# Kernel tuning notes

Hardware: AMD Instinct MI355X
Metric: run time of the kernel (lower is better)

The kernel has to match this reference:

```python
import jax, jax.numpy as jnp
import numpy as np

EMB, ENC, HID, L, V = 512, 1024, 1024, 2, 32000
INTER = (HID + ENC + EMB + V) // 16  # 2160, matches int((h+i+e+v)/16)
B, S_ENC, T_DEC = 32, 64, 64


def setup_inputs() -> dict:
    key = jax.random.key(0)
    ks = jax.random.split(key, 24)
    w = lambda k, shape, fan: (jax.random.normal(k, shape, jnp.float32) / np.sqrt(fan))
    inp = {
        'enc_output': jax.random.normal(ks[0], (B, S_ENC, ENC), jnp.float32),
        'encoder_mask': jnp.ones((B, S_ENC), jnp.int32),
        'y_input': jax.random.randint(ks[1], (B, T_DEC), 0, V),
        'dec_h0': jax.random.normal(ks[2], (L, B, HID), jnp.float32),
        'dec_c0': jax.random.normal(ks[3], (L, B, HID), jnp.float32),
        # embedding table
        'emb_table': w(ks[4], (V, EMB), EMB),
        # additive (Bahdanau) attention params: score = v^T tanh(We*enc + Wd*h_top)
        'We': w(ks[5], (ENC, HID), ENC),
        'Wd': w(ks[6], (HID, HID), HID),
        'v': w(ks[7], (HID,), HID),
        # 2-layer LSTM (torch gate order i,f,g,o)
        'W_ih0': w(ks[8], (4 * HID, EMB + ENC), EMB + ENC),
        'W_hh0': w(ks[9], (4 * HID, HID), HID),
        'b_ih0': jnp.zeros((4 * HID,), jnp.float32),
        'b_hh0': jnp.zeros((4 * HID,), jnp.float32),
        'W_ih1': w(ks[10], (4 * HID, HID), HID),
        'W_hh1': w(ks[11], (4 * HID, HID), HID),
        'b_ih1': jnp.zeros((4 * HID,), jnp.float32),
        'b_hh1': jnp.zeros((4 * HID,), jnp.float32),
        # output MLP head
        'out_W': w(ks[12], (INTER, HID + ENC + EMB), HID + ENC + EMB),
        'out_b': jnp.zeros((INTER,), jnp.float32),
        'sm_W': w(ks[13], (V, INTER), INTER),
        'sm_b': jnp.zeros((V,), jnp.float32),
        'teacher_forcing_ratio': 1,
    }
    return inp


def _lstm_cell(x, h, c, W_ih, W_hh, b_ih, b_hh):
    g = x @ W_ih.T + b_ih + h @ W_hh.T + b_hh
    i, f, gg, o = jnp.split(g, 4, axis=-1)
    c2 = jax.nn.sigmoid(f) * c + jax.nn.sigmoid(i) * jnp.tanh(gg)
    h2 = jax.nn.sigmoid(o) * jnp.tanh(c2)
    return h2, c2


def reference(enc_output, encoder_mask, y_input, dec_h0, dec_c0, emb_table,
              We, Wd, v, W_ih0, W_hh0, b_ih0, b_hh0, W_ih1, W_hh1, b_ih1, b_hh1,
              out_W, out_b, sm_W, sm_b, teacher_forcing_ratio):
    # teacher_forcing_ratio == 1 -> always use ground-truth previous token
    embs = emb_table[y_input[:, :-1]]            # [B, T-1, E] (dropout p=0 -> identity)
    enc_proj = jnp.einsum('bse,eh->bsh', enc_output, We)  # precomputed attention key proj
    mask = encoder_mask.astype(bool)
    neg = jnp.float32(-1e9)

    def step(carry, emb_t):
        h, c = carry                              # each [L, B, H]
        # additive attention over encoder states using top-layer decoder h
        score = jnp.einsum('bsh,h->bs', jnp.tanh(enc_proj + (h[-1] @ Wd)[:, None, :]), v)
        w_att = jax.nn.softmax(jnp.where(mask, score, neg), axis=-1)  # [B, S]
        ctx = jnp.einsum('bs,bsd->bd', w_att, enc_output)             # [B, ENC]
        x = jnp.concatenate([emb_t, ctx], axis=-1)                    # [B, E+ENC]
        h0, c0 = _lstm_cell(x, h[0], c[0], W_ih0, W_hh0, b_ih0, b_hh0)
        h1, c1 = _lstm_cell(h0, h[1], c[1], W_ih1, W_hh1, b_ih1, b_hh1)
        lin_in = jnp.concatenate([h1, ctx, emb_t], axis=-1)           # [B, H+ENC+E]
        logits = jnp.tanh(lin_in @ out_W.T + out_b) @ sm_W.T + sm_b   # [B, V]
        return (jnp.stack([h0, h1]), jnp.stack([c0, c1])), (logits, w_att)

    (_, _), (out_t, attw_t) = jax.lax.scan(step, (dec_h0, dec_c0), jnp.swapaxes(embs, 0, 1))
    output = jnp.swapaxes(out_t, 0, 1)            # [B, T-1, V]
    return output, attw_t                         # attw_t: [T-1, B, S]
```

## Files before the change

kernel.cpp:

```cpp
#include <hip/hip_runtime.h>
#include <hip/hip_bf16.h>

#define BB 32
#define SS 64
#define TT 63
#define EMBD 512
#define ENCD 1024
#define HIDD 1024
#define VV 32000
#define INTERD 2160
#define LIND 2560
#define TV (TT*VV)
#define OUT_ATT ((long)BB*TT*VV)

typedef float f32;
typedef unsigned short ushort_t;
typedef unsigned long long u64;
typedef __attribute__((ext_vector_type(8))) short bf16x8;
typedef __attribute__((ext_vector_type(4))) float f32x4;
typedef __attribute__((ext_vector_type(8))) unsigned short u16x8;

#define OFF_LINBF 0L
#define OFF_WD    10485760L
#define OFF_WHH0  (OFF_WD + 2097152L)
#define OFF_WIH0C (OFF_WHH0 + 8388608L)
#define OFF_WIH1  (OFF_WIH0C + 8388608L)
#define OFF_WHH1  (OFF_WIH1 + 8388608L)
#define OFF_WEND  (OFF_WHH1 + 8388608L)
#define OFF_EG    OFF_WEND
#define OFF_ENCF  OFF_EG
#define OFF_WET   (OFF_EG + 4194304L)
#define OFF_SMCH  OFF_EG
#define OFF_EPB   (OFF_EG + 16777216L)
#define OFF_EOB   (OFF_EPB + 4194304L)
#define OFF_EMBF  (OFF_EOB + 4194304L)
#define OFF_HWD   (OFF_EMBF + 2097152L)
#define OFF_C0    (OFF_HWD + 131072L)
#define OFF_C1    (OFF_C0 + 131072L)
#define OFF_CNT   (OFF_C1 + 131072L)
#define OFF_H0B   (OFF_CNT + 4096L)
#define OFF_H1B   (OFF_H0B + 4194304L)
#define OFF_CXB   (OFF_H1B + 4194304L)
#define OFF_HIDBF OFF_WD

__device__ __forceinline__ f32 fast_tanh(f32 x){
    f32 e = __expf(2.0f*x);
    return 1.0f - 2.0f/(e+1.0f);
}
__device__ __forceinline__ f32 fast_sig(f32 x){
    return 1.0f/(1.0f+__expf(-x));
}
__device__ __forceinline__ ushort_t f2bf(f32 x){
    __hip_bfloat16 h = __float2bfloat16(x);
    return *(ushort_t*)&h;
}
__device__ __forceinline__ f32 bf2f(ushort_t u){
    unsigned v = ((unsigned)u) << 16;
    return __uint_as_float(v);
}
__device__ __forceinline__ void uc_st8(u64* p, u64 v){
  __hip_atomic_store(p, v, __ATOMIC_RELAXED, __HIP_MEMORY_SCOPE_AGENT);
}
__device__ __forceinline__ void uc_st4f(f32* p, f32 v){
  __hip_atomic_store(p, v, __ATOMIC_RELAXED, __HIP_MEMORY_SCOPE_AGENT);
}
__device__ __forceinline__ void uc_st2(ushort_t* p, ushort_t v){
  __hip_atomic_store(p, v, __ATOMIC_RELAXED, __HIP_MEMORY_SCOPE_AGENT);
}

__device__ __forceinline__ long frag_idx(int row, int k, int nkt){
  return (((long)((row>>4)*nkt + (k>>5)))<<9) + ((row&15) + (((k&31)>>3)<<4))*8 + (k&7);
}

__global__ void k_setup(const f32* __restrict__ c0in, f32* __restrict__ cst,
                        unsigned* __restrict__ cnt){
  int g = blockIdx.x*256 + threadIdx.x;
  if(g < 2*BB*HIDD) cst[g] = c0in[g];
  if(g < 128) cnt[g] = 0;
}

__global__ void k_fill_emb(const f32* __restrict__ emb_table, const int* __restrict__ y,
                           ushort_t* __restrict__ embf, ushort_t* __restrict__ lin_bf){
  int i = blockIdx.x*256 + threadIdx.x;
  if(i >= TT*BB*EMBD) return;
  int e = i & (EMBD-1);
  int tb = i >> 9; int b = tb & 31; int t = tb >> 5;
  int tok = y[b*64 + t];
  ushort_t bv = f2bf(emb_table[(long)tok*EMBD + e]);
  int row = t*32 + b;
  embf[frag_idx(row, e, 16)] = bv;
  lin_bf[frag_idx(row, 2048 + e, 80)] = bv;
}

__global__ void k_cast_eo(const f32* __restrict__ eo, ushort_t* __restrict__ eob){
  int i = blockIdx.x*256 + threadIdx.x;
  if(i < BB*SS*ENCD) eob[i] = f2bf(eo[i]);
}

__global__ void k_conv(const f32* __restrict__ src, ushort_t* __restrict__ dst,
                       int ld, int rows, int kmax, int nkt, long ntiles, int tr, int perm){
  long g = (long)blockIdx.x*256 + threadIdx.x;
  long tile = g >> 6;
  if(tile >= ntiles) return;
  int lane = (int)(g & 63);
  int kt = (int)(tile % nkt);
  int rsub = (int)(tile / nkt);
  int r = rsub*16 + (lane&15);
  int k0 = kt*32 + ((lane>>4)<<3);
  int rs = perm ? ((r&3)*1024 + (r>>2)) : r;
  u16x8 v;
  if(!tr && r < rows && (k0+8) <= kmax){
    float4 a = *(const float4*)(src + (long)rs*ld + k0);
    float4 b = *(const float4*)(src + (long)rs*ld + k0 + 4);
    v[0]=f2bf(a.x); v[1]=f2bf(a.y); v[2]=f2bf(a.z); v[3]=f2bf(a.w);
    v[4]=f2bf(b.x); v[5]=f2bf(b.y); v[6]=f2bf(b.z); v[7]=f2bf(b.w);
  } else {
    #pragma unroll
    for(int j=0;j<8;j++){
      int k = k0+j;
      f32 x = 0.f;
      if(r < rows && k < kmax) x = tr ? src[(long)k*ld + rs] : src[(long)rs*ld + k];
      v[j] = f2bf(x);
    }
  }
  *(u16x8*)(dst + (tile<<9) + lane*8) = v;
}

__global__ __launch_bounds__(256)
void k_mfma_ep(const ushort_t* __restrict__ At, const ushort_t* __restrict__ Bt,
               ushort_t* __restrict__ Cout){
  const int tid = threadIdx.x, wid = tid >> 6, lane = tid & 63;
  const int wm = wid >> 1, wn = wid & 1;
  const int bm = blockIdx.x, bn = blockIdx.y;
  f32x4 acc[4][4] = {};
  for(int kt=0; kt<32; ++kt){
    bf16x8 af[4], bfr[4];
    #pragma unroll
    for(int i=0;i<4;i++){
      af[i]  = *(const bf16x8*)(At + (((long)(bm*8 + wm*4 + i)*32 + kt)<<9) + lane*8);
      bfr[i] = *(const bf16x8*)(Bt + (((long)(bn*8 + wn*4 + i)*32 + kt)<<9) + lane*8);
    }
    #pragma unroll
    for(int mi=0;mi<4;mi++)
      #pragma unroll
      for(int ni=0;ni<4;ni++)
        acc[mi][ni] = __builtin_amdgcn_mfma_f32_16x16x32_bf16(af[mi], bfr[ni], acc[mi][ni], 0, 0, 0);
  }
  #pragma unroll
  for(int mi=0;mi<4;mi++)
    #pragma unroll
    for(int ni=0;ni<4;ni++)
      #pragma unroll
      for(int r=0;r<4;r++){
        int gm = bm*128 + wm*64 + mi*16 + (lane>>4)*4 + r;
        int gn = bn*128 + wn*64 + ni*16 + (lane&15);
        Cout[(long)gm*1024 + gn] = f2bf(acc[mi][ni][r]);
      }
}

template<int NKT>
__global__ __launch_bounds__(256)
void k_logits(const ushort_t* __restrict__ At, const ushort_t* __restrict__ Bt,
              const f32* __restrict__ bias, f32* __restrict__ out, int n0){
  const int tid = threadIdx.x, wid = tid >> 6, lane = tid & 63;
  const int wm = wid >> 1, wn = wid & 1;
  const int bm = blockIdx.x, bn = blockIdx.y;
  f32x4 acc[4][4] = {};
  for(int kt=0; kt<NKT; ++kt){
    bf16x8 af[4], bfr[4];
    #pragma unroll
    for(int i=0;i<4;i++){
      af[i]  = *(const bf16x8*)(At + (((long)(bm*8 + wm*4 + i)*NKT + kt)<<9) + lane*8);
      bfr[i] = *(const bf16x8*)(Bt + (((long)(bn*8 + wn*4 + i)*NKT + kt)<<9) + lane*8);
    }
    #pragma unroll
    for(int mi=0;mi<4;mi++)
      #pragma unroll
      for(int ni=0;ni<4;ni++)
        acc[mi][ni] = __builtin_amdgcn_mfma_f32_16x16x32_bf16(af[mi], bfr[ni], acc[mi][ni], 0, 0, 0);
  }
  #pragma unroll
  for(int mi=0;mi<4;mi++)
    #pragma unroll
    for(int ni=0;ni<4;ni++)
      #pragma unroll
      for(int r=0;r<4;r++){
        int gm = bm*128 + wm*64 + mi*16 + (lane>>4)*4 + r;
        int gn = bn*128 + wn*64 + ni*16 + (lane&15);
        if(gm < TT*BB){
          int tt = gm >> 5, b = gm & 31;
          out[(long)b*TV + (long)tt*VV + n0 + gn] = acc[mi][ni][r] + bias[gn];
        }
      }
}

__device__ __forceinline__ void stage64(ushort_t* Ash, const ushort_t* src, int tid){
  __syncthreads();
  const f32x4* s = (const f32x4*)src;
  f32x4* d = (f32x4*)Ash;
  #pragma unroll
  for(int c=0;c<16;c++) d[c*256 + tid] = s[c*256 + tid];
  __syncthreads();
}

__device__ __forceinline__ void gemm32(const ushort_t* __restrict__ Ash,
    const ushort_t* __restrict__ Bp, int lane, f32x4& a0, f32x4& a1){
  #pragma unroll 4
  for(int kt=0;kt<32;kt++){
    bf16x8 b  = *(const bf16x8*)(Bp + (kt<<9) + lane*8);
    bf16x8 x0 = *(const bf16x8*)(Ash + (kt<<9) + lane*8);
    bf16x8 x1 = *(const bf16x8*)(Ash + 16384 + (kt<<9) + lane*8);
    a0 = __builtin_amdgcn_mfma_f32_16x16x32_bf16(x0, b, a0, 0, 0, 0);
    a1 = __builtin_amdgcn_mfma_f32_16x16x32_bf16(x1, b, a1, 0, 0, 0);
  }
}

__device__ __forceinline__ void gbar(unsigned* __restrict__ cnt, unsigned target,
                                     int tid, int blk){
  asm volatile("s_waitcnt vmcnt(0)" ::: "memory");
  __syncthreads();
  if(tid == 0)
    __hip_atomic_fetch_add(&cnt[(blk & 7)*16], 1u,
                           __ATOMIC_RELAXED, __HIP_MEMORY_SCOPE_AGENT);
  if(tid < 64){
    for(;;){
      unsigned v = (tid < 8) ? __hip_atomic_load(&cnt[tid*16],
                       __ATOMIC_RELAXED, __HIP_MEMORY_SCOPE_AGENT) : 0u;
      v += __shfl_xor(v, 1); v += __shfl_xor(v, 2); v += __shfl_xor(v, 4);
      unsigned tot = __shfl(v, 0);
      if(tot >= target) break;
      __builtin_amdgcn_s_sleep(2);
    }
  }
  __syncthreads();
}

__device__ __forceinline__ void cell_half(const f32x4& acc, int bhalf, int lane,
    int ns, int j, f32 bia, const ushort_t* eg_t,
    f32* __restrict__ cst, ushort_t* __restrict__ hdst, ushort_t* __restrict__ ldst){
  int q = (lane&15)&3;
  #pragma unroll
  for(int r=0;r<4;r++){
    int b = bhalf*16 + ((lane>>4)<<2) + r;
    f32 v = acc[r] + bia;
    if(eg_t) v += bf2f(eg_t[(((long)b)<<12) + ns*16 + (lane&15)]);
    f32 x1 = __shfl_xor(v,1), x2 = __shfl_xor(v,2), x3 = __shfl_xor(x1,2);
    f32 gi = q==0? v : q==1? x1 : q==2? x2 : x3;
    f32 gf = q==0? x1: q==1? v  : q==2? x3 : x2;
    f32 gg = q==0? x2: q==1? x3 : q==2? v  : x1;
    f32 go = q==0? x3: q==1? x2 : q==2? x1 : v;
    f32 cold = cst[b*HIDD + j];
    f32 cc = fast_sig(gf)*cold + fast_sig(gi)*fast_tanh(gg);
    f32 hh = fast_sig(go)*fast_tanh(cc);
    if(q == 0){
      cst[b*HIDD + j] = cc;
      ushort_t hb = f2bf(hh);
      uc_st2(hdst + frag_idx(b, j, 32), hb);
      if(ldst) ldst[frag_idx(b, j, 80)] = hb;
    }
  }
}

__global__ __launch_bounds__(256, 1)
void k_loop(char* __restrict__ ws, const f32* __restrict__ vvec,
            const int* __restrict__ maskp,
            const f32* __restrict__ b_ih0, const f32* __restrict__ b_hh0,
            const f32* __restrict__ b_ih1, const f32* __restrict__ b_hh1,
            f32* __restrict__ out){
  ushort_t* lin_bf = (ushort_t*)(ws + OFF_LINBF);
  const ushort_t* Wdt   = (const ushort_t*)(ws + OFF_WD);
  const ushort_t* Whh0f = (const ushort_t*)(ws + OFF_WHH0);
  const ushort_t* Wih0cf= (const ushort_t*)(ws + OFF_WIH0C);
  const ushort_t* Wih1f = (const ushort_t*)(ws + OFF_WIH1);
  const ushort_t* Whh1f = (const ushort_t*)(ws + OFF_WHH1);
  const ushort_t* eg    = (const ushort_t*)(ws + OFF_EG);
  const ushort_t* epb   = (const ushort_t*)(ws + OFF_EPB);
  const ushort_t* eob   = (const ushort_t*)(ws + OFF_EOB);
  f32* hwd = (f32*)(ws + OFF_HWD);
  f32* c0  = (f32*)(ws + OFF_C0);
  f32* c1  = (f32*)(ws + OFF_C1);
  ushort_t* h0b = (ushort_t*)(ws + OFF_H0B);
  ushort_t* h1b = (ushort_t*)(ws + OFF_H1B);
  ushort_t* cxb = (ushort_t*)(ws + OFF_CXB);
  unsigned* cnt  = (unsigned*)(ws + OFF_CNT);
  f32* attw = out + OUT_ATT;

  const int tid = threadIdx.x, wid = tid >> 6, lane = tid & 63;
  const int blk = blockIdx.x;
  const int gw = blk*4 + wid;
  const int ns = gw;
  const int jj = (lane&15)>>2;
  const int q0 = (lane&15)&3;
  const int jcol = ns*4 + jj;
  const int bidx = q0*HIDD + jcol;

  __shared__ __align__(16) ushort_t Ash[32768];
  __shared__ f32 hwS[HIDD];
  __shared__ f32 vvS[HIDD];
  __shared__ f32 scs[SS];
  __shared__ f32 wsm[SS];

  for(int i=tid;i<HIDD;i+=256) vvS[i] = vvec[i];

  const f32 bia0 = b_ih0[bidx] + b_hh0[bidx];
  const f32 bia1 = b_ih1[bidx] + b_hh1[bidx];

  stage64(Ash, h0b, tid);
  f32x4 g0a = {0.f,0.f,0.f,0.f}, g0b = {0.f,0.f,0.f,0.f};
  gemm32(Ash, Whh0f + ((long)ns<<14), lane, g0a, g0b);

  unsigned bar = 0;
  for(int t=0; t<TT; ++t){
    stage64(Ash, h1b + (long)t*32768, tid);
    f32x4 g1a = {0.f,0.f,0.f,0.f}, g1b = {0.f,0.f,0.f,0.f};
    gemm32(Ash, Whh1f + ((long)ns<<14), lane, g1a, g1b);
    if(gw < 64){
      f32x4 da = {0.f,0.f,0.f,0.f}, db = {0.f,0.f,0.f,0.f};
      gemm32(Ash, Wdt + ((long)gw<<14), lane, da, db);
      int col = gw*16 + (lane&15), r0 = (lane>>4)*4;
      #pragma unroll
      for(int r=0;r<4;r++){
        uc_st4f(&hwd[(r0+r)*HIDD + col], da[r]);
        uc_st4f(&hwd[(16+r0+r)*HIDD + col], db[r]);
      }
    }
    bar += 64; gbar(cnt, bar, tid, blk);

    if(blk < 32){
      int b = blk;
      {
        f32x4 hv;
        const f32* hp = hwd + b*HIDD + tid*4;
        asm volatile("global_load_dwordx4 %0, %1, off sc0 sc1\n\ts_waitcnt vmcnt(0)"
                     : "=v"(hv) : "v"(hp) : "memory");
        *(f32x4*)&hwS[tid*4] = hv;
      }
      __syncthreads();
      #pragma unroll 1
      for(int si=0; si<16; ++si){
        int s = wid*16 + si;
        const ushort_t* ep = epb + ((long)(b*SS+s)<<10) + lane*16;
        u16x8 e0 = *(const u16x8*)ep;
        u16x8 e1 = *(const u16x8*)(ep+8);
        f32 p = 0.f;
        #pragma unroll
        for(int j=0;j<8;j++)
          p = __builtin_fmaf(vvS[lane*16+j], fast_tanh(bf2f(e0[j]) + hwS[lane*16+j]), p);
        #pragma unroll
        for(int j=0;j<8;j++)
          p = __builtin_fmaf(vvS[lane*16+8+j], fast_tanh(bf2f(e1[j]) + hwS[lane*16+8+j]), p);
        #pragma unroll
        for(int off=32; off; off>>=1) p += __shfl_down(p, off);
        if(lane == 0) scs[s] = p;
      }
      __syncthreads();
      if(tid < 64){
        int s = tid;
        f32 x = maskp[b*SS+s] ? scs[s] : -1e9f;
        f32 m = x;
        #pragma unroll
        for(int off=32; off; off>>=1) m = fmaxf(m, __shfl_xor(m, off));
        f32 e = __expf(x - m);
        f32 sum = e;
        #pragma unroll
        for(int off=32; off; off>>=1) sum += __shfl_xor(sum, off);
        f32 w = e/sum;
        wsm[s] = w;
        attw[(long)t*(BB*SS) + b*SS + s] = w;
      }
      __syncthreads();
      if(tid < 128){
        int d0 = tid*8;
        f32 a[8] = {0.f,0.f,0.f,0.f,0.f,0.f,0.f,0.f};
        const ushort_t* eo = eob + ((long)b<<16) + d0;
        #pragma unroll 8
        for(int s=0;s<SS;s++){
          u16x8 v = *(const u16x8*)(eo + ((long)s<<10));
          f32 w = wsm[s];
          #pragma unroll
          for(int j=0;j<8;j++) a[j] = __builtin_fmaf(w, bf2f(v[j]), a[j]);
        }
        u16x8 cf;
        #pragma unroll
        for(int j=0;j<8;j++) cf[j] = f2bf(a[j]);
        u64 lo = (u64)(unsigned short)cf[0] | ((u64)(unsigned short)cf[1]<<16)
               | ((u64)(unsigned short)cf[2]<<32) | ((u64)(unsigned short)cf[3]<<48);
        u64 hi = (u64)(unsigned short)cf[4] | ((u64)(unsigned short)cf[5]<<16)
               | ((u64)(unsigned short)cf[6]<<32) | ((u64)(unsigned short)cf[7]<<48);
        long fi = frag_idx(b, d0, 32);
        ushort_t* cx_t = cxb + (long)t*32768;
        uc_st8((u64*)(cx_t + fi), lo);
        uc_st8((u64*)(cx_t + fi + 4), hi);
        *(u16x8*)(lin_bf + (long)t*81920 + frag_idx(b, 1024 + d0, 80)) = cf;
      }
    }
    bar += 64; gbar(cnt, bar, tid, blk);

    stage64(Ash, cxb + (long)t*32768, tid);
    gemm32(Ash, Wih0cf + ((long)ns<<14), lane, g0a, g0b);
    {
      const ushort_t* eg_t = eg + (((long)(t*BB))<<12);
      ushort_t* h0_t = h0b + (long)(t+1)*32768;
      cell_half(g0a, 0, lane, ns, jcol, bia0, eg_t, c0, h0_t, (ushort_t*)nullptr);
      cell_half(g0b, 1, lane, ns, jcol, bia0, eg_t, c0, h0_t, (ushort_t*)nullptr);
    }
    bar += 64; gbar(cnt, bar, tid, blk);

    stage64(Ash, h0b + (long)(t+1)*32768, tid);
    gemm32(Ash, Wih1f + ((long)ns<<14), lane, g1a, g1b);
    {
      ushort_t* h1_t = h1b + (long)(t+1)*32768;
      ushort_t* lt = lin_bf + (long)t*81920;
      cell_half(g1a, 0, lane, ns, jcol, bia1, (const ushort_t*)nullptr, c1, h1_t, lt);
      cell_half(g1b, 1, lane, ns, jcol, bia1, (const ushort_t*)nullptr, c1, h1_t, lt);
    }
    g0a = (f32x4){0.f,0.f,0.f,0.f}; g0b = (f32x4){0.f,0.f,0.f,0.f};
    gemm32(Ash, Whh0f + ((long)ns<<14), lane, g0a, g0b);
    bar += 64; gbar(cnt, bar, tid, blk);
  }
}

template<int NKT, int EPI, bool PERM>
__global__ __launch_bounds__(256)
void k_mfma2(const ushort_t* __restrict__ At, const f32* __restrict__ B,
             int ldb, int nrowsB, int kmaxB,
             const f32* __restrict__ bias, void* __restrict__ Cout){
  const int tid = threadIdx.x, wid = tid >> 6, lane = tid & 63;
  const int wm = wid >> 1, wn = wid & 1;
  const int bm = blockIdx.x, bn = blockIdx.y;
  f32x4 acc[4][4] = {};
  const int rbase = bn*128 + wn*64 + (lane&15);
  const int kb = (lane>>4)*8;
  for(int kt=0; kt<NKT; ++kt){
    bf16x8 af[4], bfr[4];
    #pragma unroll
    for(int i=0;i<4;i++)
      af[i] = *(const bf16x8*)(At + (((long)(bm*8 + wm*4 + i)*NKT + kt)<<9) + lane*8);
    int k0 = kt*32 + kb;
    #pragma unroll
    for(int i=0;i<4;i++){
      int r = rbase + i*16;
      int rs = PERM ? ((r&3)*1024 + (r>>2)) : r;
      u16x8 v;
      if(r < nrowsB && (k0+8) <= kmaxB){
        float4 x = *(const float4*)(B + (long)rs*ldb + k0);
        float4 y = *(const float4*)(B + (long)rs*ldb + k0 + 4);
        v[0]=f2bf(x.x); v[1]=f2bf(x.y); v[2]=f2bf(x.z); v[3]=f2bf(x.w);
        v[4]=f2bf(y.x); v[5]=f2bf(y.y); v[6]=f2bf(y.z); v[7]=f2bf(y.w);
      } else {
        #pragma unroll
        for(int j=0;j<8;j++){
          int k = k0+j;
          f32 xx = (r < nrowsB && k < kmaxB) ? B[(long)rs*ldb + k] : 0.f;
          v[j] = f2bf(xx);
        }
      }
      bfr[i] = *(bf16x8*)&v;
    }
    #pragma unroll
    for(int mi=0;mi<4;mi++)
      #pragma unroll
      for(int ni=0;ni<4;ni++)
        acc[mi][ni] = __builtin_amdgcn_mfma_f32_16x16x32_bf16(af[mi], bfr[ni], acc[mi][ni], 0, 0, 0);
  }
  #pragma unroll
  for(int mi=0;mi<4;mi++){
    #pragma unroll
    for(int ni=0;ni<4;ni++){
      #pragma unroll
      for(int r=0;r<4;r++){
        int gm = bm*128 + wm*64 + mi*16 + (lane>>4)*4 + r;
        int gn = bn*128 + wn*64 + ni*16 + (lane&15);
        f32 x = acc[mi][ni][r];
        if(EPI == 1){
          x = (gn < INTERD) ? fast_tanh(x + bias[gn]) : 0.f;
          ushort_t* hb = (ushort_t*)Cout;
          int msub = gm >> 4, ktile = gn >> 5;
          int lane_a = (gm & 15) + (((gn & 31) >> 3) << 4);
          hb[(((long)(msub*68 + ktile)) << 9) + lane_a*8 + (gn & 7)] = f2bf(x);
        } else {
          ((ushort_t*)Cout)[((long)gm<<12) + gn] = f2bf(x);
        }
      }
    }
  }
}

extern "C" void kernel_launch(void* const* d_in, const int* in_sizes, int n_in,
                              void* d_out, int out_size, void* d_ws, size_t ws_size,
                              hipStream_t stream){
  (void)in_sizes; (void)n_in; (void)out_size; (void)ws_size;
  const f32* enc_output = (const f32*)d_in[0];
  const int* mask  = (const int*)d_in[1];
  const int* y     = (const int*)d_in[2];
  const f32* dec_h0= (const f32*)d_in[3];
  const f32* dec_c0= (const f32*)d_in[4];
  const f32* emb   = (const f32*)d_in[5];
  const f32* We    = (const f32*)d_in[6];
  const f32* Wd    = (const f32*)d_in[7];
  const f32* vvec  = (const f32*)d_in[8];
  const f32* W_ih0 = (const f32*)d_in[9];
  const f32* W_hh0 = (const f32*)d_in[10];
  const f32* b_ih0 = (const f32*)d_in[11];
  const f32* b_hh0 = (const f32*)d_in[12];
  const f32* W_ih1 = (const f32*)d_in[13];
  const f32* W_hh1 = (const f32*)d_in[14];
  const f32* b_ih1 = (const f32*)d_in[15];
  const f32* b_hh1 = (const f32*)d_in[16];
  const f32* out_W = (const f32*)d_in[17];
  const f32* out_b = (const f32*)d_in[18];
  const f32* sm_W  = (const f32*)d_in[19];
  const f32* sm_b  = (const f32*)d_in[20];
  f32* out = (f32*)d_out;
  char* ws = (char*)d_ws;

  ushort_t* lin_bf = (ushort_t*)(ws + OFF_LINBF);
  ushort_t* epb = (ushort_t*)(ws + OFF_EPB);
  ushort_t* eob = (ushort_t*)(ws + OFF_EOB);
  ushort_t* encf  = (ushort_t*)(ws + OFF_ENCF);
  ushort_t* wetf  = (ushort_t*)(ws + OFF_WET);
  ushort_t* embf  = (ushort_t*)(ws + OFF_EMBF);
  ushort_t* egbuf = (ushort_t*)(ws + OFF_EG);
  ushort_t* smch  = (ushort_t*)(ws + OFF_SMCH);
  ushort_t* hid_bf = (ushort_t*)(ws + OFF_HIDBF);

  k_setup<<<dim3(256), dim3(256), 0, stream>>>(dec_c0, (f32*)(ws + OFF_C0),
                                               (unsigned*)(ws + OFF_CNT));
  k_fill_emb<<<dim3(4032), dim3(256), 0, stream>>>(emb, y, embf, lin_bf);
  k_conv<<<dim3(1024), dim3(256), 0, stream>>>(enc_output, encf, ENCD, BB*SS, ENCD, 32, 128L*32, 0, 0);
  k_conv<<<dim3(512),  dim3(256), 0, stream>>>(We,         wetf, HIDD, HIDD,  ENCD, 32, 64L*32, 1, 0);
  k_mfma_ep<<<dim3(16,8), dim3(256), 0, stream>>>(encf, wetf, epb);
  k_cast_eo<<<dim3(8192), dim3(256), 0, stream>>>(enc_output, eob);

  k_mfma2<16,3,true><<<dim3(16,32), dim3(256), 0, stream>>>(
      embf, W_ih0, 1536, 4096, 512, (const f32*)nullptr, egbuf);

  k_conv<<<dim3(512),  dim3(256), 0, stream>>>(Wd,        (ushort_t*)(ws+OFF_WD),    HIDD, HIDD, HIDD, 32, 64L*32, 1, 0);
  k_conv<<<dim3(2048), dim3(256), 0, stream>>>(W_hh0,     (ushort_t*)(ws+OFF_WHH0),  HIDD, 4096, HIDD, 32, 256L*32, 0, 1);
  k_conv<<<dim3(2048), dim3(256), 0, stream>>>(W_ih0+512, (ushort_t*)(ws+OFF_WIH0C), 1536, 4096, HIDD, 32, 256L*32, 0, 1);
  k_conv<<<dim3(2048), dim3(256), 0, stream>>>(W_ih1,     (ushort_t*)(ws+OFF_WIH1),  HIDD, 4096, HIDD, 32, 256L*32, 0, 1);
  k_conv<<<dim3(2048), dim3(256), 0, stream>>>(W_hh1,     (ushort_t*)(ws+OFF_WHH1),  HIDD, 4096, HIDD, 32, 256L*32, 0, 1);
  k_conv<<<dim3(16),   dim3(256), 0, stream>>>(dec_h0,       (ushort_t*)(ws+OFF_H0B), HIDD, BB, HIDD, 32, 64, 0, 0);
  k_conv<<<dim3(16),   dim3(256), 0, stream>>>(dec_h0+32768, (ushort_t*)(ws+OFF_H1B), HIDD, BB, HIDD, 32, 64, 0, 0);

  k_loop<<<dim3(64), dim3(256), 0, stream>>>(ws, vvec, mask,
      b_ih0, b_hh0, b_ih1, b_hh1, out);

  k_mfma2<80,1,false><<<dim3(16,17), dim3(256), 0, stream>>>(
      lin_bf, out_W, LIND, INTERD, LIND, out_b, hid_bf);
  for(int c=0; c<8; ++c){
    int n0 = c*4096;
    int rows = (c<7) ? 4096 : 3328;
    int nsub = rows >> 4;
    long ntiles = (long)nsub*68;
    k_conv<<<dim3((unsigned)((ntiles*64+255)/256)), dim3(256), 0, stream>>>(
        sm_W + (long)n0*INTERD, smch, INTERD, rows, INTERD, 68, ntiles, 0, 0);
    k_logits<68><<<dim3(16, nsub/8), dim3(256), 0, stream>>>(
        hid_bf, smch, sm_b + n0, out, n0);
  }
}
```

Before: 4.950 ms.

## Repartition persistent LSTM loop by batch half and two gate slices per wave

The persistent recurrence kernel now splits its 64 blocks into two batch halves times 32 column groups. Each wave computes two 16-column gate slices against a 16-row batch half, so each block stages only half the activation tile into shared memory and the attention projection work is spread across column groups. Hidden-state stores are packed into 8-byte writes through lane shuffles instead of scalar 2-byte atomic stores. It also adds nontemporal loads and stores and shortens the barrier sleep. The trade-off is twice as many weight fragment loads per activation fragment, since each wave now reads two weight slices instead of one.

```diff
diff --git a/kernel.cpp b/kernel.cpp
--- a/kernel.cpp
+++ b/kernel.cpp
@@ -64,9 +64,6 @@
 __device__ __forceinline__ void uc_st4f(f32* p, f32 v){
   __hip_atomic_store(p, v, __ATOMIC_RELAXED, __HIP_MEMORY_SCOPE_AGENT);
 }
-__device__ __forceinline__ void uc_st2(ushort_t* p, ushort_t v){
-  __hip_atomic_store(p, v, __ATOMIC_RELAXED, __HIP_MEMORY_SCOPE_AGENT);
-}
 
 __device__ __forceinline__ long frag_idx(int row, int k, int nkt){
   return (((long)((row>>4)*nkt + (k>>5)))<<9) + ((row&15) + (((k&31)>>3)<<4))*8 + (k&7);
@@ -194,24 +191,34 @@
       }
 }
 
-__device__ __forceinline__ void stage64(ushort_t* Ash, const ushort_t* src, int tid){
+__device__ __forceinline__ void stage32(ushort_t* Ash, const ushort_t* src, int tid){
   __syncthreads();
   const f32x4* s = (const f32x4*)src;
   f32x4* d = (f32x4*)Ash;
   #pragma unroll
-  for(int c=0;c<16;c++) d[c*256 + tid] = s[c*256 + tid];
+  for(int c=0;c<8;c++) d[c*256 + tid] = __builtin_nontemporal_load(&s[c*256 + tid]);
   __syncthreads();
 }
 
-__device__ __forceinline__ void gemm32(const ushort_t* __restrict__ Ash,
-    const ushort_t* __restrict__ Bp, int lane, f32x4& a0, f32x4& a1){
+__device__ __forceinline__ void gemm2(const ushort_t* __restrict__ Ash,
+    const ushort_t* __restrict__ B0, const ushort_t* __restrict__ B1, int lane,
+    f32x4& a0, f32x4& a1){
   #pragma unroll 4
   for(int kt=0;kt<32;kt++){
-    bf16x8 b  = *(const bf16x8*)(Bp + (kt<<9) + lane*8);
-    bf16x8 x0 = *(const bf16x8*)(Ash + (kt<<9) + lane*8);
-    bf16x8 x1 = *(const bf16x8*)(Ash + 16384 + (kt<<9) + lane*8);
-    a0 = __builtin_amdgcn_mfma_f32_16x16x32_bf16(x0, b, a0, 0, 0, 0);
-    a1 = __builtin_amdgcn_mfma_f32_16x16x32_bf16(x1, b, a1, 0, 0, 0);
+    bf16x8 x  = *(const bf16x8*)(Ash + (kt<<9) + lane*8);
+    bf16x8 b0 = *(const bf16x8*)(B0 + (kt<<9) + lane*8);
+    bf16x8 b1 = *(const bf16x8*)(B1 + (kt<<9) + lane*8);
+    a0 = __builtin_amdgcn_mfma_f32_16x16x32_bf16(x, b0, a0, 0, 0, 0);
+    a1 = __builtin_amdgcn_mfma_f32_16x16x32_bf16(x, b1, a1, 0, 0, 0);
+  }
+}
+__device__ __forceinline__ void gemm1(const ushort_t* __restrict__ Ash,
+    const ushort_t* __restrict__ B0, int lane, f32x4& a0){
+  #pragma unroll 4
+  for(int kt=0;kt<32;kt++){
+    bf16x8 x  = *(const bf16x8*)(Ash + (kt<<9) + lane*8);
+    bf16x8 b0 = *(const bf16x8*)(B0 + (kt<<9) + lane*8);
+    a0 = __builtin_amdgcn_mfma_f32_16x16x32_bf16(x, b0, a0, 0, 0, 0);
   }
 }
 
@@ -229,21 +236,23 @@
       v += __shfl_xor(v, 1); v += __shfl_xor(v, 2); v += __shfl_xor(v, 4);
       unsigned tot = __shfl(v, 0);
       if(tot >= target) break;
-      __builtin_amdgcn_s_sleep(2);
+      __builtin_amdgcn_s_sleep(1);
     }
   }
   __syncthreads();
 }
 
-__device__ __forceinline__ void cell_half(const f32x4& acc, int bhalf, int lane,
-    int ns, int j, f32 bia, const ushort_t* eg_t,
-    f32* __restrict__ cst, ushort_t* __restrict__ hdst, ushort_t* __restrict__ ldst){
-  int q = (lane&15)&3;
+__device__ __forceinline__ void cell_ns(const f32x4& acc, int bg, int ns, int lane,
+    f32 bia, const ushort_t* eg_t, f32* __restrict__ cst,
+    ushort_t* __restrict__ hdst, ushort_t* __restrict__ ldst){
+  const int q = (lane&15)&3;
+  const int j = ns*4 + ((lane&15)>>2);
+  f32 hv[4];
   #pragma unroll
   for(int r=0;r<4;r++){
-    int b = bhalf*16 + ((lane>>4)<<2) + r;
+    int b = bg*16 + ((lane>>4)<<2) + r;
     f32 v = acc[r] + bia;
-    if(eg_t) v += bf2f(eg_t[(((long)b)<<12) + ns*16 + (lane&15)]);
+    if(eg_t) v += bf2f(__builtin_nontemporal_load(eg_t + (((long)b)<<12) + ns*16 + (lane&15)));
     f32 x1 = __shfl_xor(v,1), x2 = __shfl_xor(v,2), x3 = __shfl_xor(x1,2);
     f32 gi = q==0? v : q==1? x1 : q==2? x2 : x3;
     f32 gf = q==0? x1: q==1? v  : q==2? x3 : x2;
@@ -252,11 +261,22 @@
     f32 cold = cst[b*HIDD + j];
     f32 cc = fast_sig(gf)*cold + fast_sig(gi)*fast_tanh(gg);
     f32 hh = fast_sig(go)*fast_tanh(cc);
-    if(q == 0){
-      cst[b*HIDD + j] = cc;
-      ushort_t hb = f2bf(hh);
-      uc_st2(hdst + frag_idx(b, j, 32), hb);
-      if(ldst) ldst[frag_idx(b, j, 80)] = hb;
+    if(q == 0) cst[b*HIDD + j] = cc;
+    hv[r] = hh;
+  }
+  const int Lbase = lane & 48;
+  #pragma unroll
+  for(int r=0;r<4;r++){
+    f32 h0_ = __shfl(hv[r], Lbase);
+    f32 h1_ = __shfl(hv[r], Lbase+4);
+    f32 h2_ = __shfl(hv[r], Lbase+8);
+    f32 h3_ = __shfl(hv[r], Lbase+12);
+    if((lane & 15) == 0){
+      u64 pk = (u64)f2bf(h0_) | ((u64)f2bf(h1_)<<16)
+             | ((u64)f2bf(h2_)<<32) | ((u64)f2bf(h3_)<<48);
+      int b = bg*16 + ((lane>>4)<<2) + r;
+      uc_st8((u64*)(hdst + frag_idx(b, ns*4, 32)), pk);
+      if(ldst) __builtin_nontemporal_store(pk, (u64*)(ldst + frag_idx(b, ns*4, 80)));
     }
   }
 }
@@ -287,14 +307,12 @@
 
   const int tid = threadIdx.x, wid = tid >> 6, lane = tid & 63;
   const int blk = blockIdx.x;
-  const int gw = blk*4 + wid;
-  const int ns = gw;
-  const int jj = (lane&15)>>2;
-  const int q0 = (lane&15)&3;
-  const int jcol = ns*4 + jj;
-  const int bidx = q0*HIDD + jcol;
-
-  __shared__ __align__(16) ushort_t Ash[32768];
+  const int bg  = blk >> 5;
+  const int cg  = blk & 31;
+  const int ns0 = cg*8 + wid*2, ns1 = ns0 + 1;
+  const long hoff = (long)bg*16384;
+
+  __shared__ __align__(16) ushort_t Ash[16384];
   __shared__ f32 hwS[HIDD];
   __shared__ f32 vvS[HIDD];
   __shared__ f32 scs[SS];
@@ -302,26 +320,31 @@
 
   for(int i=tid;i<HIDD;i+=256) vvS[i] = vvec[i];
 
-  const f32 bia0 = b_ih0[bidx] + b_hh0[bidx];
-  const f32 bia1 = b_ih1[bidx] + b_hh1[bidx];
-
-  stage64(Ash, h0b, tid);
+  const int q0_ = (lane&15)&3;
+  const int j0 = ns0*4 + ((lane&15)>>2), j1 = ns1*4 + ((lane&15)>>2);
+  const f32 bia00 = b_ih0[q0_*HIDD + j0] + b_hh0[q0_*HIDD + j0];
+  const f32 bia01 = b_ih0[q0_*HIDD + j1] + b_hh0[q0_*HIDD + j1];
+  const f32 bia10 = b_ih1[q0_*HIDD + j0] + b_hh1[q0_*HIDD + j0];
+  const f32 bia11 = b_ih1[q0_*HIDD + j1] + b_hh1[q0_*HIDD + j1];
+
+  stage32(Ash, h0b + hoff, tid);
   f32x4 g0a = {0.f,0.f,0.f,0.f}, g0b = {0.f,0.f,0.f,0.f};
-  gemm32(Ash, Whh0f + ((long)ns<<14), lane, g0a, g0b);
+  gemm2(Ash, Whh0f + ((long)ns0<<14), Whh0f + ((long)ns1<<14), lane, g0a, g0b);
 
   unsigned bar = 0;
   for(int t=0; t<TT; ++t){
-    stage64(Ash, h1b + (long)t*32768, tid);
+    stage32(Ash, h1b + (long)t*32768 + hoff, tid);
     f32x4 g1a = {0.f,0.f,0.f,0.f}, g1b = {0.f,0.f,0.f,0.f};
-    gemm32(Ash, Whh1f + ((long)ns<<14), lane, g1a, g1b);
-    if(gw < 64){
-      f32x4 da = {0.f,0.f,0.f,0.f}, db = {0.f,0.f,0.f,0.f};
-      gemm32(Ash, Wdt + ((long)gw<<14), lane, da, db);
-      int col = gw*16 + (lane&15), r0 = (lane>>4)*4;
+    gemm2(Ash, Whh1f + ((long)ns0<<14), Whh1f + ((long)ns1<<14), lane, g1a, g1b);
+    if(wid < 2){
+      int td = cg*2 + wid;
+      f32x4 da = {0.f,0.f,0.f,0.f};
+      gemm1(Ash, Wdt + ((long)td<<14), lane, da);
+      int col = td*16 + (lane&15);
       #pragma unroll
       for(int r=0;r<4;r++){
-        uc_st4f(&hwd[(r0+r)*HIDD + col], da[r]);
-        uc_st4f(&hwd[(16+r0+r)*HIDD + col], db[r]);
+        int b = bg*16 + ((lane>>4)<<2) + r;
+        uc_st4f(&hwd[b*HIDD + col], da[r]);
       }
     }
     bar += 64; gbar(cnt, bar, tid, blk);
@@ -391,31 +414,34 @@
         ushort_t* cx_t = cxb + (long)t*32768;
         uc_st8((u64*)(cx_t + fi), lo);
         uc_st8((u64*)(cx_t + fi + 4), hi);
-        *(u16x8*)(lin_bf + (long)t*81920 + frag_idx(b, 1024 + d0, 80)) = cf;
+        __builtin_nontemporal_store(*(u64*)&lo,
+            (u64*)(lin_bf + (long)t*81920 + frag_idx(b, 1024 + d0, 80)));
+        __builtin_nontemporal_store(*(u64*)&hi,
+            (u64*)(lin_bf + (long)t*81920 + frag_idx(b, 1024 + d0 + 4, 80)));
       }
     }
     bar += 64; gbar(cnt, bar, tid, blk);
 
-    stage64(Ash, cxb + (long)t*32768, tid);
-    gemm32(Ash, Wih0cf + ((long)ns<<14), lane, g0a, g0b);
+    stage32(Ash, cxb + (long)t*32768 + hoff, tid);
+    gemm2(Ash, Wih0cf + ((long)ns0<<14), Wih0cf + ((long)ns1<<14), lane, g0a, g0b);
     {
       const ushort_t* eg_t = eg + (((long)(t*BB))<<12);
       ushort_t* h0_t = h0b + (long)(t+1)*32768;
-      cell_half(g0a, 0, lane, ns, jcol, bia0, eg_t, c0, h0_t, (ushort_t*)nullptr);
-      cell_half(g0b, 1, lane, ns, jcol, bia0, eg_t, c0, h0_t, (ushort_t*)nullptr);
+      cell_ns(g0a, bg, ns0, lane, bia00, eg_t, c0, h0_t, (ushort_t*)nullptr);
+      cell_ns(g0b, bg, ns1, lane, bia01, eg_t, c0, h0_t, (ushort_t*)nullptr);
     }
     bar += 64; gbar(cnt, bar, tid, blk);
 
-    stage64(Ash, h0b + (long)(t+1)*32768, tid);
-    gemm32(Ash, Wih1f + ((long)ns<<14), lane, g1a, g1b);
+    stage32(Ash, h0b + (long)(t+1)*32768 + hoff, tid);
+    gemm2(Ash, Wih1f + ((long)ns0<<14), Wih1f + ((long)ns1<<14), lane, g1a, g1b);
     {
       ushort_t* h1_t = h1b + (long)(t+1)*32768;
       ushort_t* lt = lin_bf + (long)t*81920;
-      cell_half(g1a, 0, lane, ns, jcol, bia1, (const ushort_t*)nullptr, c1, h1_t, lt);
-      cell_half(g1b, 1, lane, ns, jcol, bia1, (const ushort_t*)nullptr, c1, h1_t, lt);
+      cell_ns(g1a, bg, ns0, lane, bia10, (const ushort_t*)nullptr, c1, h1_t, lt);
+      cell_ns(g1b, bg, ns1, lane, bia11, (const ushort_t*)nullptr, c1, h1_t, lt);
     }
     g0a = (f32x4){0.f,0.f,0.f,0.f}; g0b = (f32x4){0.f,0.f,0.f,0.f};
-    gemm32(Ash, Whh0f + ((long)ns<<14), lane, g0a, g0b);
+    gemm2(Ash, Whh0f + ((long)ns0<<14), Whh0f + ((long)ns1<<14), lane, g0a, g0b);
     bar += 64; gbar(cnt, bar, tid, blk);
   }
 }
```

New measurement: 5.661 ms. 1.14x slower.
